# Kernel optimization log

Hardware: AMD Instinct MI355X
Metric: run time of the kernel (lower is better)

Reference implementation:

```python
import jax, jax.numpy as jnp
import numpy as np

# constants matching KernelBAE: scl=1 (initialize), beta=penalty=0.01, temp passed to EStep, steps=1
SCL = 1.0
BETA = 0.01
TEMP = 0.5
STEPS = 1
N, M = 4096, 128


def setup_inputs() -> dict:
    key = jax.random.key(0)
    kK, kS, kU = jax.random.split(key, 3)
    G = jax.random.normal(kK, (N, N), dtype=jnp.float32)
    K = 0.5 * (G + G.T)  # symmetric kernel-like matrix (self.data)
    S = (jax.random.uniform(kS, (N, M)) < 0.25).astype(jnp.float32)
    u = jax.random.uniform(kU, (N, M), dtype=jnp.float32)  # Gibbs uniforms, one per (row, feature)
    perm = jnp.arange(N, dtype=jnp.int32)  # row visit order
    return {"K": K, "S": S, "u": u, "perm": perm}


def _gibbs(K, S, u, perm):
    """Faithful translation of update_concepts_kernel: sequential per-row Gibbs
    sweep of binary codes with rank-one StS/St1 updates."""
    n, m = S.shape
    nf = jnp.asarray(n, S.dtype)
    t = (nf - 1.0) / nf

    StS0 = S.T @ S          # (m, m)
    St10 = S.sum(0)         # (m,)

    def row_step(carry, xs):
        S, StS, St1 = carry
        i, u_row = xs
        k_row = K[i]                      # (n,) row of kernel
        k0 = k_row[i]
        s = S[i]                          # current code of row i
        # S[I].T @ K[i, I] == S.T @ K[i] - s * K[i,i]
        Sk = S.T @ k_row - s * k0
        # rank-one downdate (remove row i)
        St1 = St1 - s
        StS = StS - jnp.outer(s, s)

        D1 = StS
        D2 = St1[None, :] - StS
        D3 = St1[:, None] - StS
        D4 = (nf - 1.0) - St1[None, :] - St1[:, None] + StS
        b1 = ((D1 < D2) & (D1 < D3) & (D1 < D4)).astype(S.dtype)
        b2 = ((D2 < D1) & (D2 < D3) & (D2 < D4)).astype(S.dtype)
        b3 = ((D3 < D2) & (D3 < D1) & (D3 < D4)).astype(S.dtype)
        b4 = ((D4 < D2) & (D4 < D3) & (D4 < D1)).astype(S.dtype)
        R = b1 - b2 - b3 + b4             # (m, m)
        r = b2.sum(0) - b4.sum(0)         # (m,)

        s_ = St1 / (nf - 1.0)
        uv = 2.0 * s_ - 1.0
        ssc = s_ * (1.0 - s_)
        sx0 = s_ @ (s - s_)
        ux0 = 2.0 * sx0 - s.sum() + s_.sum()
        h = t * (SCL ** 2 * ssc.sum() - SCL * k0) * uv + 2.0 * SCL * Sk - BETA * SCL ** 2 * r
        Jii = 2.0 * (nf - 1.0) * ssc + t * uv ** 2

        def elem(c, xs2):
            news, sx, ux = c
            j, uj = xs2
            dot = (2.0 * (StS[j] @ (news - s_))
                   - 2.0 * (nf - 1.0) * s_[j] * sx
                   + t * uv[j] * ux
                   - Jii[j] * news[j]
                   + BETA * (R[j] @ news))
            curr = (h[j] - SCL ** 2 * Jii[j] / 2.0 - SCL ** 2 * dot) / TEMP
            prob = jnp.where(curr < -100.0, 0.0,
                             jnp.where(curr > 100.0, 1.0, jax.nn.sigmoid(curr)))
            sj = (uj < prob).astype(news.dtype)
            ds = sj - news[j]
            news = news.at[j].set(sj)
            return (news, sx + ds * s_[j], ux + ds * uv[j]), None

        js = jnp.tile(jnp.arange(m, dtype=jnp.int32), STEPS)
        us = jnp.tile(u_row, STEPS)
        (news, _, _), _ = jax.lax.scan(elem, (s, sx0, ux0), (js, us))

        S = S.at[i].set(news)
        return (S, StS + jnp.outer(news, news), St1 + news), None

    (S, _, _), _ = jax.lax.scan(row_step, (S, StS0, St10), (perm, u))
    return S


_gibbs_jit = jax.jit(_gibbs)


def reference(K, S, u, perm):
    # EStep (Gibbs sweep) followed by the module's __call__: scl * S @ S.T
    Snew = _gibbs_jit(K, S, u, perm)
    return SCL * (Snew @ Snew.T)
```

## Files before the change

kernel.cpp:

```cpp
#include <hip/hip_runtime.h>
#include <math.h>

typedef unsigned long long u64;
typedef unsigned int u32;

#define NN 4096
#define MM 128

#define OFF_PCT 0
#define OFF_LG  4194304
#define OFF_RM  8388608
#define OFF_CM  8454144
#define OFF_STS 8519680
#define OFF_ST1 8585216
#define TAILB   67043328

__global__ void k_pack_rows(const float* __restrict__ S, u64* __restrict__ RM) {
  int lane = threadIdx.x & 63;
  int w = blockIdx.x * 4 + (threadIdx.x >> 6);
  for (int rr = 0; rr < 16; ++rr) {
    int row = w * 16 + rr;
    u64 m0 = __ballot(S[(size_t)row * MM + lane] > 0.5f);
    u64 m1 = __ballot(S[(size_t)row * MM + 64 + lane] > 0.5f);
    if (lane == 0) { RM[row * 2] = m0; RM[row * 2 + 1] = m1; }
  }
}

__global__ void k_pack_cols(const float* __restrict__ S, u64* __restrict__ CM) {
  int lane = threadIdx.x & 63;
  int w = blockIdx.x * 4 + (threadIdx.x >> 6);
  for (int k = 0; k < 64; ++k) {
    int pair = w * 64 + k;
    int j = pair >> 6, wd = pair & 63;
    u64 m = __ballot(S[((size_t)wd * 64 + lane) * MM + j] > 0.5f);
    if (lane == 0) CM[j * 64 + wd] = m;
  }
}

__global__ void k_init_sts(const u64* __restrict__ CM, int* __restrict__ StSg,
                           int* __restrict__ St1g) {
  int id = blockIdx.x * 256 + threadIdx.x;
  int a = id >> 7, b = id & 127;
  int s = 0;
  for (int w = 0; w < 64; ++w) s += __popcll(CM[a * 64 + w] & CM[b * 64 + w]);
  StSg[a * 128 + b] = s;
  if (a == b) St1g[a] = s;
}

__global__ void k_logit(const float* __restrict__ U, double* __restrict__ Lg) {
  int idx = blockIdx.x * 256 + threadIdx.x;
  float u = U[idx];
  double L = (u <= 0.0f) ? -1e300 : log((double)u / (1.0 - (double)u));
  Lg[idx] = L;
}

__global__ void k_pgemm(const float* __restrict__ K, const float* __restrict__ S,
                        double* __restrict__ PCT) {
  __shared__ float Slds[64 * 128];
  __shared__ float Klds[64 * 16];
  int tid = threadIdx.x;
  int col0 = blockIdx.x * 16;
  int c = tid & 15, jg = tid >> 4;
  int j0 = jg * 8;
  double acc[8];
#pragma unroll
  for (int q = 0; q < 8; ++q) acc[q] = 0.0;
  for (int rb = 0; rb < NN; rb += 64) {
    for (int k = 0; k < 32; ++k)
      Slds[k * 256 + tid] = S[(size_t)rb * MM + k * 256 + tid];
    for (int k = 0; k < 4; ++k) {
      int idx = k * 256 + tid;
      int rr = idx >> 4, cc = idx & 15;
      Klds[idx] = K[(size_t)(rb + rr) * NN + col0 + cc];
    }
    __syncthreads();
    for (int rr = 0; rr < 64; ++rr) {
      double kv = (double)Klds[rr * 16 + c];
#pragma unroll
      for (int q = 0; q < 8; ++q)
        acc[q] += (double)Slds[rr * 128 + j0 + q] * kv;
    }
    __syncthreads();
  }
#pragma unroll
  for (int q = 0; q < 8; ++q)
    PCT[(size_t)(col0 + c) * MM + j0 + q] = acc[q];
}

__global__ void k_cgemm(const float* __restrict__ K, const int* __restrict__ perm,
                        const float* __restrict__ S, const u64* __restrict__ RMg,
                        double* __restrict__ PCT, int blk) {
  __shared__ float sDD[128 * 128];
  __shared__ float sDk[128 * 16];
  int tid = threadIdx.x;
  int col0 = blockIdx.x * 16;
  int base = blk * 128;
  for (int k = 0; k < 64; ++k) {
    int e = k * 256 + tid;
    int tp = e >> 7, j = e & 127;
    int pj = perm[base + tp];
    u64 w = RMg[(size_t)pj * 2 + (j >> 6)];
    int nb = (int)((w >> (j & 63)) & 1);
    int sb = (S[(size_t)pj * MM + j] > 0.5f) ? 1 : 0;
    sDD[e] = (float)(nb - sb);
  }
  if (tid < 128) {
    int pj = perm[base + tid];
    for (int cc = 0; cc < 16; ++cc)
      sDk[tid * 16 + cc] = K[(size_t)pj * NN + col0 + cc];
  }
  __syncthreads();
  int c = tid & 15, jg = tid >> 4;
  int j0 = jg * 8;
  double acc[8];
#pragma unroll
  for (int q = 0; q < 8; ++q) acc[q] = 0.0;
  for (int tp = 0; tp < 128; ++tp) {
    double kv = (double)sDk[tp * 16 + c];
#pragma unroll
    for (int q = 0; q < 8; ++q)
      acc[q] += (double)sDD[tp * 128 + j0 + q] * kv;
  }
#pragma unroll
  for (int q = 0; q < 8; ++q) {
    size_t o = (size_t)(col0 + c) * MM + j0 + q;
    PCT[o] += acc[q];
  }
}

__global__ __launch_bounds__(1024) void k_seq(const float* __restrict__ Kg,
                                              const int* __restrict__ perm,
                                              char* scratch, int blk) {
  if (blockIdx.x != 0) {
    if (threadIdx.x < 256) {
      float a = 1.0001f + (float)threadIdx.x, b = 1.0002f, c = 1.0003f, d = 1.0004f;
      for (int i = 0; i < 120000; ++i) {
        a = __builtin_fmaf(a, 1.000001f, 0.0001f);
        b = __builtin_fmaf(b, 1.000001f, 0.0001f);
        c = __builtin_fmaf(c, 1.000001f, 0.0001f);
        d = __builtin_fmaf(d, 1.000001f, 0.0001f);
      }
      asm volatile("" :: "v"(a), "v"(b), "v"(c), "v"(d));
    }
    return;
  }

  __shared__ int sStS[128 * 129];
  __shared__ signed char sDT[128 * 144];
  __shared__ int4 rI[1024];
  __shared__ double rC[1024];
  __shared__ int sSt1b[2][128];
  __shared__ double sKcD[2][128], sPCb[2][128], sLb[2][128];
  __shared__ int sPerm[128];
  __shared__ u64 sBM[128][2];
  __shared__ u64 sPrevN[2];

  const int tid = threadIdx.x;
  int* StSg = (int*)(scratch + OFF_STS);
  int* St1g = (int*)(scratch + OFF_ST1);
  double* PCT = (double*)(scratch + OFF_PCT);
  double* Lg = (double*)(scratch + OFF_LG);
  u64* RMg = (u64*)(scratch + OFF_RM);
  const int base = blk * 128;

  for (int k = 0; k < 16; ++k) {
    int idx = k * 1024 + tid;
    int a = idx >> 7, b = idx & 127;
    sStS[a * 129 + b] = StSg[idx];
  }
  for (int idx = tid; idx < 128 * 144 / 4; idx += 1024) ((int*)sDT)[idx] = 0;
  int pjReg = 0;
  float regK = 0.f;
  double regPC = 0.0, regL = 0.0;
  if (tid < 128) {
    int pj = perm[base + tid];
    sPerm[tid] = pj;
    sSt1b[1][tid] = St1g[tid];
    sBM[tid][0] = RMg[(size_t)pj * 2];
    sBM[tid][1] = RMg[(size_t)pj * 2 + 1];
  }
  if (tid >= 128 && tid < 256) {
    int e = tid - 128;
    int pj = perm[base + e];
    pjReg = pj;
    int r0 = perm[base];
    sKcD[0][e] = (double)Kg[(size_t)pj * NN + r0];
    sPCb[0][e] = PCT[(size_t)r0 * MM + e];
    sLb[0][e] = Lg[(size_t)base * MM + e];
  }
  if (tid == 0) { sPrevN[0] = 0; sPrevN[1] = 0; }
  __syncthreads();

  for (int t = 0; t < 128; ++t) {
    const int wb = t & 1, rb = (t + 1) & 1;
    {
      if (t < 127 && tid >= 128 && tid < 256) {
        int e = tid - 128;
        int rn = sPerm[t + 1];
        regK = Kg[(size_t)pjReg * NN + rn];
        regPC = PCT[(size_t)rn * MM + e];
        regL = Lg[(size_t)(base + t + 1) * MM + e];
      }
      const int j = tid & 127;
      const int g = tid >> 7;
      u64 pn0 = sPrevN[0], pn1 = sPrevN[1];
      u64 cs0 = sBM[t][0], cs1 = sBM[t][1];
      int pbj = (int)(((j < 64 ? pn0 : pn1) >> (j & 63)) & 1);
      int obj = (int)(((j < 64 ? cs0 : cs1) >> (j & 63)) & 1);
      int q = sSt1b[rb][j] + pbj - obj;
      if (g == 0) sSt1b[wb][j] = q;
      unsigned rowP = (unsigned)(((g < 4 ? pn0 : pn1) >> ((g & 3) * 16)) & 0xFFFFull);
      unsigned rowO = (unsigned)(((g < 4 ? cs0 : cs1) >> ((g & 3) * 16)) & 0xFFFFull);
      int pk[16];
      {
        const int4* p4 = (const int4*)(&sSt1b[rb][g * 16]);
        int4 a = p4[0], b = p4[1], c = p4[2], d = p4[3];
        pk[0] = a.x; pk[1] = a.y; pk[2] = a.z; pk[3] = a.w;
        pk[4] = b.x; pk[5] = b.y; pk[6] = b.z; pk[7] = b.w;
        pk[8] = c.x; pk[9] = c.y; pk[10] = c.z; pk[11] = c.w;
        pk[12] = d.x; pk[13] = d.y; pk[14] = d.z; pk[15] = d.w;
      }
#pragma unroll
      for (int k = 0; k < 16; ++k)
        pk[k] += (int)((rowP >> k) & 1) - (int)((rowO >> k) & 1);
      double kcd[16];
#pragma unroll
      for (int k = 0; k < 16; ++k) kcd[k] = sKcD[wb][g * 16 + k];
      int dw[4];
      {
        const int4* d4 = (const int4*)(sDT + j * 144 + g * 16);
        int4 v = d4[0];
        dw[0] = v.x; dw[1] = v.y; dw[2] = v.z; dw[3] = v.w;
      }
      int cq = 4095 - q;
      int myP1 = 0, myRR = 0, myr = 0, myQ = 0;
      double myC = 0.0;
#pragma unroll
      for (int k = 0; k < 16; ++k) {
        int off = (g * 16 + k) * 129 + j;
        int x = sStS[off];
        int nA = (int)((rowP >> k) & 1), oA = (int)((rowO >> k) & 1);
        int dlt = (nA & pbj) - (oA & obj);
        if (dlt) { x += dlt; sStS[off] = x; }
        int p = pk[k];
        int y = x + x;
        int w = y + cq - p;
        int b2 = (q < y) & (q < p) & (q < w);
        int b4 = (w < y) & (w < p) & (w < q);
        myr += b2 - b4;
        if (oA) {
          int b1 = (y < p) & (y < q) & (y < w);
          int b3 = (p < y) & (p < q) & (p < w);
          myRR += b1 - b2 - b3 + b4;
          myP1 += x;
        }
        myQ += x * p;
        int dv = (dw[k >> 2] << (24 - (k & 3) * 8)) >> 24;
        myC += (double)dv * kcd[k];
      }
      int o = g * 128 + j;
      rI[o] = make_int4(myP1, myRR, myr, myQ);
      rC[o] = myC;
    }
    __syncthreads();
    if (tid >= 128 && tid < 256 && t < 127) {
      int e = tid - 128;
      sKcD[rb][e] = (double)regK;
      sPCb[rb][e] = regPC;
      sLb[rb][e] = regL;
    }
    if (tid < 64) {
      const int l = tid;
      int st0i = sSt1b[wb][l], st1i = sSt1b[wb][l + 64];
      int P1i0 = 0, P1i1 = 0, RRi0 = 0, RRi1 = 0, rv0 = 0, rv1 = 0;
      long long Q0l = 0, Q1l = 0;
      double C0s = 0.0, C1s = 0.0;
#pragma unroll
      for (int g2 = 0; g2 < 8; ++g2) {
        int4 v0 = rI[g2 * 128 + l];
        int4 v1 = rI[g2 * 128 + 64 + l];
        P1i0 += v0.x; RRi0 += v0.y; rv0 += v0.z; Q0l += (long long)v0.w;
        P1i1 += v1.x; RRi1 += v1.y; rv1 += v1.z; Q1l += (long long)v1.w;
        C0s += rC[g2 * 128 + l];
        C1s += rC[g2 * 128 + 64 + l];
      }
      double st0d = (double)st0i, st1d = (double)st1i;
      double Q0 = (double)Q0l, Q1 = (double)Q1l;
      u64 um0 = sBM[t][0], um1 = sBM[t][1];
      int sb0 = (int)((um0 >> l) & 1), sb1 = (int)((um1 >> l) & 1);
      double k0d = sKcD[wb][t];
      double Sk0 = sPCb[wb][l] + C0s - (sb0 ? k0d : 0.0);
      double Sk1 = sPCb[wb][l + 64] + C1s - (sb1 ? k0d : 0.0);
      const double cc = 4095.0;
      const double tt = 4095.0 / 4096.0;
      double s_0 = st0d / cc, s_1 = st1d / cc;
      double uv0 = 2.0 * s_0 - 1.0, uv1 = 2.0 * s_1 - 1.0;
      double ssc0 = s_0 * (1.0 - s_0), ssc1 = s_1 * (1.0 - s_1);
      double Jii0 = 2.0 * cc * ssc0 + tt * uv0 * uv0;
      double Jii1 = 2.0 * cc * ssc1 + tt * uv1 * uv1;
      double sscS = ssc0 + ssc1;
      double SSv = st0d * st0d + st1d * st1d;
      double S1v = st0d + st1d;
      int SNi = st0i * sb0 + st1i * sb1;
#pragma unroll
      for (int o = 1; o < 64; o <<= 1) {
        sscS += __shfl_xor(sscS, o);
        SSv += __shfl_xor(SSv, o);
        S1v += __shfl_xor(S1v, o);
        SNi += __shfl_xor(SNi, o);
      }
      int Nni = __popcll(um0) + __popcll(um1);
      double h0 = tt * (sscS - k0d) * uv0 + 2.0 * Sk0 - 0.01 * (double)rv0;
      double h1 = tt * (sscS - k0d) * uv1 + 2.0 * Sk1 - 0.01 * (double)rv1;
      double c2 = cc * cc;
      double SSc2 = SSv / c2, S1sc = S1v / cc;
      double C00 = 2.0 * h0 - Jii0 + 4.0 * Q0 / cc + 4.0 * SSc2 * (tt * uv0 - st0d) - 2.0 * tt * uv0 * S1sc;
      double C01 = 2.0 * h1 - Jii1 + 4.0 * Q1 / cc + 4.0 * SSc2 * (tt * uv1 - st1d) - 2.0 * tt * uv1 * S1sc;
      double C10 = (4.0 / cc) * (st0d - tt * uv0), C11 = (4.0 / cc) * (st1d - tt * uv1);
      double C20 = 2.0 * tt * uv0, C21 = 2.0 * tt * uv1;
      double JT0 = 2.0 * Jii0, JT1 = 2.0 * Jii1;
      double L0 = sLb[wb][l], L1 = sLb[wb][l + 64];
      double E0 = C00 + C10 * (double)SNi + C20 * (double)Nni + (sb0 ? JT0 : 0.0);
      double E1 = C01 + C11 * (double)SNi + C21 * (double)Nni + (sb1 ? JT1 : 0.0);
      double CUR0 = E0 - 4.0 * (double)P1i0 - 0.02 * (double)RRi0;
      double CUR1 = E1 - 4.0 * (double)P1i1 - 0.02 * (double)RRi1;
      u64 nm0 = um0, nm1 = um1;
      const int* sSt1w = sSt1b[wb];
      int jmin = 0;
      while (jmin < 128) {
        int d0 = (CUR0 > 100.0) || ((CUR0 >= -100.0) && (L0 < CUR0));
        int d1 = (CUR1 > 100.0) || ((CUR1 >= -100.0) && (L1 < CUR1));
        u64 w0 = __ballot(d0) ^ nm0;
        u64 w1 = __ballot(d1) ^ nm1;
        if (jmin < 64) {
          w0 &= (~0ull) << jmin;
        } else {
          w0 = 0;
          w1 &= (~0ull) << (jmin - 64);
        }
        int jj;
        if (w0) jj = __builtin_ctzll(w0);
        else if (w1) jj = 64 + __builtin_ctzll(w1);
        else break;
        int x0 = sStS[jj * 129 + l];
        int x1 = sStS[jj * 129 + 64 + l];
        int stc = sSt1w[jj];
        int slot = jj >> 6, bpos = jj & 63;
        int ob = (int)(((slot ? nm1 : nm0) >> bpos) & 1);
        int R0, R1;
        {
          int y = x0 + x0, w = y + (4095 - st0i) - stc;
          int b1 = (y < stc) & (y < st0i) & (y < w);
          int b2 = (st0i < y) & (st0i < stc) & (st0i < w);
          int b3 = (stc < y) & (stc < st0i) & (stc < w);
          int b4 = (w < y) & (w < stc) & (w < st0i);
          R0 = b1 - b2 - b3 + b4;
        }
        {
          int y = x1 + x1, w = y + (4095 - st1i) - stc;
          int b1 = (y < stc) & (y < st1i) & (y < w);
          int b2 = (st1i < y) & (st1i < stc) & (st1i < w);
          int b3 = (stc < y) & (stc < st1i) & (stc < w);
          int b4 = (w < y) & (w < stc) & (w < st1i);
          R1 = b1 - b2 - b3 + b4;
        }
        double stcd = (double)stc;
        double aj = ob ? -stcd : stcd;
        double bC20 = ob ? -C20 : C20;
        double bC21 = ob ? -C21 : C21;
        double nb02 = ob ? 0.02 : -0.02;
        double W0 = aj * C10 + bC20;
        double W1 = aj * C11 + bC21;
        if (jj == l)      W0 += (ob ? -JT0 : JT0);
        if (jj == 64 + l) W1 += (ob ? -JT1 : JT1);
        double t0d = (double)(200 * x0 + R0);
        double t1d = (double)(200 * x1 + R1);
        CUR0 += W0 + nb02 * t0d;
        CUR1 += W1 + nb02 * t1d;
        if (slot) nm1 ^= 1ull << bpos; else nm0 ^= 1ull << bpos;
        jmin = jj + 1;
      }
      int nb0 = (int)((nm0 >> l) & 1), nb1 = (int)((nm1 >> l) & 1);
      sDT[l * 144 + t] = (signed char)(nb0 - sb0);
      sDT[(l + 64) * 144 + t] = (signed char)(nb1 - sb1);
      if (l == 0) {
        sPrevN[0] = nm0; sPrevN[1] = nm1;
        sBM[t][0] = nm0; sBM[t][1] = nm1;
      }
    }
    __syncthreads();
  }

  u64 fn0 = sPrevN[0], fn1 = sPrevN[1];
  for (int k = 0; k < 16; ++k) {
    int idx = k * 1024 + tid;
    int a = idx >> 7, b = idx & 127;
    int na = (int)(((a < 64 ? fn0 : fn1) >> (a & 63)) & 1);
    int nb = (int)(((b < 64 ? fn0 : fn1) >> (b & 63)) & 1);
    StSg[idx] = sStS[a * 129 + b] + (na & nb);
  }
  if (tid < 128) {
    int nb = (int)((((tid < 64) ? fn0 : fn1) >> (tid & 63)) & 1);
    St1g[tid] = sSt1b[1][tid] + nb;
    RMg[(size_t)sPerm[tid] * 2] = sBM[tid][0];
    RMg[(size_t)sPerm[tid] * 2 + 1] = sBM[tid][1];
  }
}

__global__ void k_copy_tail(char* scratch, float* out) {
  u64* TM = (u64*)((char*)out + TAILB);
  const u64* RM = (const u64*)(scratch + OFF_RM);
  int tid = threadIdx.x;
  for (int k = 0; k < 16; ++k) TM[k * 512 + tid] = RM[k * 512 + tid];
}

__global__ void k_out_main(float* __restrict__ out) {
  const u64* TM = (const u64*)((const char*)out + TAILB);
  int a = blockIdx.x;
  u64 a0 = TM[a * 2], a1 = TM[a * 2 + 1];
  int tid = threadIdx.x;
  for (int k = 0; k < 16; ++k) {
    int b = k * 256 + tid;
    u64 b0 = TM[b * 2], b1 = TM[b * 2 + 1];
    out[(size_t)a * NN + b] = (float)(__popcll(a0 & b0) + __popcll(a1 & b1));
  }
}

__global__ void k_out_tail(float* __restrict__ out) {
  __shared__ u64 sM[8192];
  const u64* TM = (const u64*)((const char*)out + TAILB);
  int tid = threadIdx.x;
  for (int k = 0; k < 8; ++k) sM[k * 1024 + tid] = TM[k * 1024 + tid];
  __syncthreads();
  for (int k = 0; k < 16; ++k) {
    int e = k * 1024 + tid;
    int a = 4092 + (e >> 12), b = e & 4095;
    out[(size_t)a * NN + b] =
        (float)(__popcll(sM[a * 2] & sM[b * 2]) + __popcll(sM[a * 2 + 1] & sM[b * 2 + 1]));
  }
}

extern "C" void kernel_launch(void* const* d_in, const int* in_sizes, int n_in,
                              void* d_out, int out_size, void* d_ws, size_t ws_size,
                              hipStream_t stream) {
  (void)in_sizes; (void)n_in; (void)out_size; (void)d_ws; (void)ws_size;
  const float* K = (const float*)d_in[0];
  const float* S = (const float*)d_in[1];
  const float* U = (const float*)d_in[2];
  const int* perm = (const int*)d_in[3];
  char* scratch = (char*)d_out;
  float* out = (float*)d_out;
  u64* RM = (u64*)(scratch + OFF_RM);
  u64* CM = (u64*)(scratch + OFF_CM);
  int* StSg = (int*)(scratch + OFF_STS);
  int* St1g = (int*)(scratch + OFF_ST1);
  double* PCT = (double*)(scratch + OFF_PCT);
  double* Lg = (double*)(scratch + OFF_LG);

  hipLaunchKernelGGL(k_pack_rows, dim3(64), dim3(256), 0, stream, S, RM);
  hipLaunchKernelGGL(k_pack_cols, dim3(32), dim3(256), 0, stream, S, CM);
  hipLaunchKernelGGL(k_init_sts, dim3(64), dim3(256), 0, stream, CM, StSg, St1g);
  hipLaunchKernelGGL(k_logit, dim3(2048), dim3(256), 0, stream, U, Lg);
  hipLaunchKernelGGL(k_pgemm, dim3(256), dim3(256), 0, stream, K, S, PCT);
  for (int b = 0; b < 32; ++b) {
    hipLaunchKernelGGL(k_seq, dim3(257), dim3(1024), 0, stream, K, perm, scratch, b);
    if (b < 31)
      hipLaunchKernelGGL(k_cgemm, dim3(256), dim3(256), 0, stream, K, perm, S,
                         (const u64*)RM, PCT, b);
  }
  hipLaunchKernelGGL(k_copy_tail, dim3(1), dim3(512), 0, stream, scratch, out);
  hipLaunchKernelGGL(k_out_main, dim3(4092), dim3(256), 0, stream, out);
  hipLaunchKernelGGL(k_out_tail, dim3(1), dim3(1024), 0, stream, out);
}
```

Baseline: 67.47 ms.

## Precompute StS/R table, prefetch inner Gibbs loop, flag-terminate dummy busy blocks

The sequential per-row Gibbs loop now reads a packed 16-bit table of StS entries and R-classification bits. The table is built during the block-parallel phase, which replaces the per-flip recomputation of R from two StS reads and St1. The next two candidate flip positions are prefetched from LDS, and St1 values come from readlane instead of shared memory. The dummy heavy-FMA blocks, which appear to keep clocks up, now spin until the main block sets a global completion flag instead of running a fixed 120000 iterations. The grid also shrinks from 257 to 256 blocks. This adds atomic polling traffic and relies on the spinning blocks being co-resident with block 0.

```diff
diff --git a/kernel.cpp b/kernel.cpp
--- a/kernel.cpp
+++ b/kernel.cpp
@@ -13,6 +13,7 @@
 #define OFF_CM  8454144
 #define OFF_STS 8519680
 #define OFF_ST1 8585216
+#define FLAG_OFF 8586240
 #define TAILB   67043328
 
 __global__ void k_pack_rows(const float* __restrict__ S, u64* __restrict__ RM) {
@@ -128,24 +129,38 @@
   }
 }
 
+#define FF1P(a, b) ((a) ? __builtin_ctzll(a) : ((b) ? 64 + __builtin_ctzll(b) : 128))
+#define CLRL(a, b) { if (a) (a) &= (a) - 1; else (b) &= (b) - 1; }
+
 __global__ __launch_bounds__(1024) void k_seq(const float* __restrict__ Kg,
                                               const int* __restrict__ perm,
                                               char* scratch, int blk) {
   if (blockIdx.x != 0) {
-    if (threadIdx.x < 256) {
-      float a = 1.0001f + (float)threadIdx.x, b = 1.0002f, c = 1.0003f, d = 1.0004f;
-      for (int i = 0; i < 120000; ++i) {
-        a = __builtin_fmaf(a, 1.000001f, 0.0001f);
-        b = __builtin_fmaf(b, 1.000001f, 0.0001f);
-        c = __builtin_fmaf(c, 1.000001f, 0.0001f);
-        d = __builtin_fmaf(d, 1.000001f, 0.0001f);
-      }
-      asm volatile("" :: "v"(a), "v"(b), "v"(c), "v"(d));
-    }
+    volatile __shared__ int sdone;
+    if (threadIdx.x == 0) sdone = 0;
+    __syncthreads();
+    int* fl = (int*)(scratch + FLAG_OFF);
+    float a = 1.0001f + (float)threadIdx.x, b = 1.0002f, c = 1.0003f, d = 1.0004f;
+    do {
+      if (threadIdx.x < 256) {
+        for (int i = 0; i < 300; ++i) {
+          a = __builtin_fmaf(a, 1.000001f, 0.0001f);
+          b = __builtin_fmaf(b, 1.000001f, 0.0001f);
+          c = __builtin_fmaf(c, 1.000001f, 0.0001f);
+          d = __builtin_fmaf(d, 1.000001f, 0.0001f);
+        }
+      } else {
+        for (int i = 0; i < 40; ++i)
+          a = __builtin_fmaf(a, 1.000001f, 0.0001f);
+      }
+      if (threadIdx.x == 0 && atomicAdd(fl, 0) > blk) sdone = 1;
+    } while (!sdone);
+    asm volatile("" :: "v"(a), "v"(b), "v"(c), "v"(d));
     return;
   }
 
   __shared__ int sStS[128 * 129];
+  __shared__ u32 sXR[128 * 64];
   __shared__ signed char sDT[128 * 144];
   __shared__ int4 rI[1024];
   __shared__ double rC[1024];
@@ -161,6 +176,7 @@
   double* PCT = (double*)(scratch + OFF_PCT);
   double* Lg = (double*)(scratch + OFF_LG);
   u64* RMg = (u64*)(scratch + OFF_RM);
+  unsigned short* sXRh = (unsigned short*)sXR;
   const int base = blk * 128;
 
   for (int k = 0; k < 16; ++k) {
@@ -237,7 +253,8 @@
       double myC = 0.0;
 #pragma unroll
       for (int k = 0; k < 16; ++k) {
-        int off = (g * 16 + k) * 129 + j;
+        int bb = g * 16 + k;
+        int off = bb * 129 + j;
         int x = sStS[off];
         int nA = (int)((rowP >> k) & 1), oA = (int)((rowO >> k) & 1);
         int dlt = (nA & pbj) - (oA & obj);
@@ -245,18 +262,18 @@
         int p = pk[k];
         int y = x + x;
         int w = y + cq - p;
+        int b1 = (y < p) & (y < q) & (y < w);
         int b2 = (q < y) & (q < p) & (q < w);
+        int b3 = (p < y) & (p < q) & (p < w);
         int b4 = (w < y) & (w < p) & (w < q);
+        int R = b1 - b2 - b3 + b4;
         myr += b2 - b4;
-        if (oA) {
-          int b1 = (y < p) & (y < q) & (y < w);
-          int b3 = (p < y) & (p < q) & (p < w);
-          myRR += b1 - b2 - b3 + b4;
-          myP1 += x;
-        }
+        if (oA) { myRR += R; myP1 += x; }
         myQ += x * p;
         int dv = (dw[k >> 2] << (24 - (k & 3) * 8)) >> 24;
         myC += (double)dv * kcd[k];
+        sXRh[(bb * 64 + (j & 63)) * 2 + (j >> 6)] =
+            (unsigned short)(x | ((R + 1) << 12));
       }
       int o = g * 128 + j;
       rI[o] = make_int4(myP1, myRR, myr, myQ);
@@ -325,60 +342,70 @@
       double CUR0 = E0 - 4.0 * (double)P1i0 - 0.02 * (double)RRi0;
       double CUR1 = E1 - 4.0 * (double)P1i1 - 0.02 * (double)RRi1;
       u64 nm0 = um0, nm1 = um1;
-      const int* sSt1w = sSt1b[wb];
-      int jmin = 0;
-      while (jmin < 128) {
-        int d0 = (CUR0 > 100.0) || ((CUR0 >= -100.0) && (L0 < CUR0));
-        int d1 = (CUR1 > 100.0) || ((CUR1 >= -100.0) && (L1 < CUR1));
-        u64 w0 = __ballot(d0) ^ nm0;
-        u64 w1 = __ballot(d1) ^ nm1;
-        if (jmin < 64) {
-          w0 &= (~0ull) << jmin;
-        } else {
-          w0 = 0;
-          w1 &= (~0ull) << (jmin - 64);
+      u64 w0, w1;
+      {
+        int d0 = (int)(CUR0 > 100.0) | ((int)(CUR0 >= -100.0) & (int)(L0 < CUR0));
+        int d1 = (int)(CUR1 > 100.0) | ((int)(CUR1 >= -100.0) & (int)(L1 < CUR1));
+        w0 = __ballot(d0) ^ nm0;
+        w1 = __ballot(d1) ^ nm1;
+      }
+      int jj = FF1P(w0, w1);
+      if (jj < 128) {
+        u64 a0c = w0, a1c = w1;
+        CLRL(a0c, a1c);
+        int jn1 = FF1P(a0c, a1c);
+        CLRL(a0c, a1c);
+        int jn2 = FF1P(a0c, a1c);
+        u32 xrC = sXR[jj * 64 + l];
+        u32 xr1 = sXR[(jn1 < 128 ? jn1 : jj) * 64 + l];
+        u32 xr2 = sXR[(jn2 < 128 ? jn2 : jj) * 64 + l];
+        for (;;) {
+          u32 xr = xrC;
+          if (jj < 64) {
+            int ob = (int)((nm0 >> jj) & 1);
+            double stcd = (double)__builtin_amdgcn_readlane(st0i, jj);
+            double T0 = (double)(200 * (int)(xr & 0xFFFu) + (int)((xr >> 12) & 3u) - 1);
+            double T1 = (double)(200 * (int)((xr >> 16) & 0xFFFu) + (int)((xr >> 28) & 3u) - 1);
+            double t0 = fma(-0.02, T0, fma(stcd, C10, C20));
+            double t1 = fma(-0.02, T1, fma(stcd, C11, C21));
+            CUR0 += (ob ? -t0 : t0) + ((l == jj) ? (ob ? -JT0 : JT0) : 0.0);
+            CUR1 += ob ? -t1 : t1;
+            nm0 ^= 1ull << jj;
+          } else {
+            int jb = jj - 64;
+            int ob = (int)((nm1 >> jb) & 1);
+            double stcd = (double)__builtin_amdgcn_readlane(st1i, jb);
+            double T1 = (double)(200 * (int)((xr >> 16) & 0xFFFu) + (int)((xr >> 28) & 3u) - 1);
+            double t1 = fma(-0.02, T1, fma(stcd, C11, C21));
+            CUR1 += (ob ? -t1 : t1) + ((l == jb) ? (ob ? -JT1 : JT1) : 0.0);
+            nm1 ^= 1ull << jb;
+          }
+          int jmin = jj + 1;
+          if (jmin < 64) {
+            int d0 = (int)(CUR0 > 100.0) | ((int)(CUR0 >= -100.0) & (int)(L0 < CUR0));
+            int d1 = (int)(CUR1 > 100.0) | ((int)(CUR1 >= -100.0) & (int)(L1 < CUR1));
+            w0 = (__ballot(d0) ^ nm0) & ((~0ull) << jmin);
+            w1 = __ballot(d1) ^ nm1;
+          } else if (jmin < 128) {
+            int d1 = (int)(CUR1 > 100.0) | ((int)(CUR1 >= -100.0) & (int)(L1 < CUR1));
+            w0 = 0;
+            w1 = (__ballot(d1) ^ nm1) & ((~0ull) << (jmin - 64));
+          } else {
+            w0 = 0; w1 = 0;
+          }
+          int nj = FF1P(w0, w1);
+          if (nj >= 128) break;
+          u32 xN = (nj == jn1) ? xr1 : ((nj == jn2) ? xr2 : sXR[nj * 64 + l]);
+          u64 b0c = w0, b1c = w1;
+          CLRL(b0c, b1c);
+          int k1 = FF1P(b0c, b1c);
+          CLRL(b0c, b1c);
+          int k2 = FF1P(b0c, b1c);
+          xr1 = sXR[(k1 < 128 ? k1 : nj) * 64 + l];
+          xr2 = sXR[(k2 < 128 ? k2 : nj) * 64 + l];
+          jn1 = k1; jn2 = k2;
+          xrC = xN; jj = nj;
         }
-        int jj;
-        if (w0) jj = __builtin_ctzll(w0);
-        else if (w1) jj = 64 + __builtin_ctzll(w1);
-        else break;
-        int x0 = sStS[jj * 129 + l];
-        int x1 = sStS[jj * 129 + 64 + l];
-        int stc = sSt1w[jj];
-        int slot = jj >> 6, bpos = jj & 63;
-        int ob = (int)(((slot ? nm1 : nm0) >> bpos) & 1);
-        int R0, R1;
-        {
-          int y = x0 + x0, w = y + (4095 - st0i) - stc;
-          int b1 = (y < stc) & (y < st0i) & (y < w);
-          int b2 = (st0i < y) & (st0i < stc) & (st0i < w);
-          int b3 = (stc < y) & (stc < st0i) & (stc < w);
-          int b4 = (w < y) & (w < stc) & (w < st0i);
-          R0 = b1 - b2 - b3 + b4;
-        }
-        {
-          int y = x1 + x1, w = y + (4095 - st1i) - stc;
-          int b1 = (y < stc) & (y < st1i) & (y < w);
-          int b2 = (st1i < y) & (st1i < stc) & (st1i < w);
-          int b3 = (stc < y) & (stc < st1i) & (stc < w);
-          int b4 = (w < y) & (w < stc) & (w < st1i);
-          R1 = b1 - b2 - b3 + b4;
-        }
-        double stcd = (double)stc;
-        double aj = ob ? -stcd : stcd;
-        double bC20 = ob ? -C20 : C20;
-        double bC21 = ob ? -C21 : C21;
-        double nb02 = ob ? 0.02 : -0.02;
-        double W0 = aj * C10 + bC20;
-        double W1 = aj * C11 + bC21;
-        if (jj == l)      W0 += (ob ? -JT0 : JT0);
-        if (jj == 64 + l) W1 += (ob ? -JT1 : JT1);
-        double t0d = (double)(200 * x0 + R0);
-        double t1d = (double)(200 * x1 + R1);
-        CUR0 += W0 + nb02 * t0d;
-        CUR1 += W1 + nb02 * t1d;
-        if (slot) nm1 ^= 1ull << bpos; else nm0 ^= 1ull << bpos;
-        jmin = jj + 1;
       }
       int nb0 = (int)((nm0 >> l) & 1), nb1 = (int)((nm1 >> l) & 1);
       sDT[l * 144 + t] = (signed char)(nb0 - sb0);
@@ -404,6 +431,10 @@
     St1g[tid] = sSt1b[1][tid] + nb;
     RMg[(size_t)sPerm[tid] * 2] = sBM[tid][0];
     RMg[(size_t)sPerm[tid] * 2 + 1] = sBM[tid][1];
+  }
+  if (tid == 0) {
+    __threadfence();
+    atomicExch((int*)(scratch + FLAG_OFF), blk + 1);
   }
 }
 
@@ -462,8 +493,9 @@
   hipLaunchKernelGGL(k_init_sts, dim3(64), dim3(256), 0, stream, CM, StSg, St1g);
   hipLaunchKernelGGL(k_logit, dim3(2048), dim3(256), 0, stream, U, Lg);
   hipLaunchKernelGGL(k_pgemm, dim3(256), dim3(256), 0, stream, K, S, PCT);
+  hipMemsetAsync(scratch + FLAG_OFF, 0, 4, stream);
   for (int b = 0; b < 32; ++b) {
-    hipLaunchKernelGGL(k_seq, dim3(257), dim3(1024), 0, stream, K, perm, scratch, b);
+    hipLaunchKernelGGL(k_seq, dim3(256), dim3(1024), 0, stream, K, perm, scratch, b);
     if (b < 31)
       hipLaunchKernelGGL(k_cgemm, dim3(256), dim3(256), 0, stream, K, perm, S,
                          (const u64*)RM, PCT, b);
```

New measurement: 75.67 ms. 1.12x slower.

## Make dummy heater blocks poll a flag so only the worker's XCC stays busy

Applied to the files above, without the earlier changes.

The sequential Gibbs kernel launches filler blocks that spin on FMAs, apparently to keep clocks or power state up while block 0 runs the serial sweep. Block 0 now writes its XCC id and block index to a global flag. Filler blocks poll that flag: those on other XCCs exit early, and those on the same XCC keep spinning until block 0 signals completion. The grid also drops from 257 to 256 blocks. This relies on clock and power behaviour and on hardware register reads, not on any algorithmic change to the computation.

```diff
diff --git a/kernel.cpp b/kernel.cpp
--- a/kernel.cpp
+++ b/kernel.cpp
@@ -13,6 +13,7 @@
 #define OFF_CM  8454144
 #define OFF_STS 8519680
 #define OFF_ST1 8585216
+#define FLAG_OFF 8586240
 #define TAILB   67043328
 
 __global__ void k_pack_rows(const float* __restrict__ S, u64* __restrict__ RM) {
@@ -128,20 +129,62 @@
   }
 }
 
+#define FF1P(a, b) ((a) ? __builtin_ctzll(a) : ((b) ? 64 + __builtin_ctzll(b) : 128))
+#define CLRL(a, b) { if (a) (a) &= (a) - 1; else (b) &= (b) - 1; }
+
+static __device__ __forceinline__ int poll_flag(int* fl) {
+  int v = 0;
+  if ((threadIdx.x & 63) == 0) v = atomicAdd(fl, 0);
+  return __builtin_amdgcn_readfirstlane(v);
+}
+
 __global__ __launch_bounds__(1024) void k_seq(const float* __restrict__ Kg,
                                               const int* __restrict__ perm,
                                               char* scratch, int blk) {
+  int xcc;
+  asm volatile("s_getreg_b32 %0, hwreg(20, 0, 32)" : "=s"(xcc));
+  int* fl = (int*)(scratch + FLAG_OFF);
+
   if (blockIdx.x != 0) {
-    if (threadIdx.x < 256) {
-      float a = 1.0001f + (float)threadIdx.x, b = 1.0002f, c = 1.0003f, d = 1.0004f;
-      for (int i = 0; i < 120000; ++i) {
+    if (threadIdx.x >= 256) return;
+    float a = 1.0001f + (float)threadIdx.x, b = 1.0002f, c = 1.0003f, d = 1.0004f;
+    for (int i = 0; i < 120000; ++i) {
+      a = __builtin_fmaf(a, 1.000001f, 0.0001f);
+      b = __builtin_fmaf(b, 1.000001f, 0.0001f);
+      c = __builtin_fmaf(c, 1.000001f, 0.0001f);
+      d = __builtin_fmaf(d, 1.000001f, 0.0001f);
+    }
+    unsigned ublk = (unsigned)blk;
+    for (;;) {
+      int v = poll_flag(fl);
+      unsigned hi = ((unsigned)v) >> 16;
+      if (hi > ublk) { asm volatile("" :: "v"(a), "v"(b), "v"(c), "v"(d)); return; }
+      if (hi == ublk && (v & 0x300)) {
+        if ((v & 0x200) || ((v & 0xFF) != (xcc & 0xFF))) {
+          asm volatile("" :: "v"(a), "v"(b), "v"(c), "v"(d));
+          return;
+        }
+        break;
+      }
+      for (int i = 0; i < 4000; ++i) {
         a = __builtin_fmaf(a, 1.000001f, 0.0001f);
         b = __builtin_fmaf(b, 1.000001f, 0.0001f);
         c = __builtin_fmaf(c, 1.000001f, 0.0001f);
         d = __builtin_fmaf(d, 1.000001f, 0.0001f);
       }
-      asm volatile("" :: "v"(a), "v"(b), "v"(c), "v"(d));
-    }
+    }
+    for (;;) {
+      for (int i = 0; i < 20000; ++i) {
+        a = __builtin_fmaf(a, 1.000001f, 0.0001f);
+        b = __builtin_fmaf(b, 1.000001f, 0.0001f);
+        c = __builtin_fmaf(c, 1.000001f, 0.0001f);
+        d = __builtin_fmaf(d, 1.000001f, 0.0001f);
+      }
+      int v = poll_flag(fl);
+      unsigned hi = ((unsigned)v) >> 16;
+      if (hi > ublk || (hi == ublk && (v & 0x200))) break;
+    }
+    asm volatile("" :: "v"(a), "v"(b), "v"(c), "v"(d));
     return;
   }
 
@@ -162,6 +205,8 @@
   double* Lg = (double*)(scratch + OFF_LG);
   u64* RMg = (u64*)(scratch + OFF_RM);
   const int base = blk * 128;
+
+  if (tid == 0) atomicExch(fl, (blk << 16) | 0x100 | (xcc & 0xFF));
 
   for (int k = 0; k < 16; ++k) {
     int idx = k * 1024 + tid;
@@ -405,6 +450,10 @@
     RMg[(size_t)sPerm[tid] * 2] = sBM[tid][0];
     RMg[(size_t)sPerm[tid] * 2 + 1] = sBM[tid][1];
   }
+  if (tid == 0) {
+    __threadfence();
+    atomicExch(fl, (blk << 16) | 0x200);
+  }
 }
 
 __global__ void k_copy_tail(char* scratch, float* out) {
@@ -462,8 +511,9 @@
   hipLaunchKernelGGL(k_init_sts, dim3(64), dim3(256), 0, stream, CM, StSg, St1g);
   hipLaunchKernelGGL(k_logit, dim3(2048), dim3(256), 0, stream, U, Lg);
   hipLaunchKernelGGL(k_pgemm, dim3(256), dim3(256), 0, stream, K, S, PCT);
+  hipMemsetAsync(scratch + FLAG_OFF, 0, 4, stream);
   for (int b = 0; b < 32; ++b) {
-    hipLaunchKernelGGL(k_seq, dim3(257), dim3(1024), 0, stream, K, perm, scratch, b);
+    hipLaunchKernelGGL(k_seq, dim3(256), dim3(1024), 0, stream, K, perm, scratch, b);
     if (b < 31)
       hipLaunchKernelGGL(k_cgemm, dim3(256), dim3(256), 0, stream, K, perm, S,
                          (const u64*)RM, PCT, b);
```

Result: slower. 75.13 ms (+11.3%).
